# Kernel optimization log

Measured on AMD Instinct MI355X. Metric: run time of the kernel, lower is better.

The kernel has to match this reference:

```python
import jax, jax.numpy as jnp
import numpy as np

N_USERS = 50000
N_ITEMS = 100000
N_NODES = N_USERS + N_ITEMS
DIM = 64
N_EDGES = 1200000
N_LAYERS = 2


def setup_inputs() -> dict:
    key = jax.random.key(0)
    k1, k2, k3, k4, k5 = jax.random.split(key, 5)
    # xavier_uniform bound for an (n, dim) embedding: sqrt(6/(n+dim)); plain normal is fine for a correctness baseline
    user_emb = jax.random.normal(k1, (N_USERS, DIM), dtype=jnp.float32)
    item_emb = jax.random.normal(k2, (N_ITEMS, DIM), dtype=jnp.float32)
    edge_rows = jax.random.randint(k3, (N_EDGES,), 0, N_NODES, dtype=jnp.int32)
    edge_cols = jax.random.randint(k4, (N_EDGES,), 0, N_NODES, dtype=jnp.int32)
    edge_vals = jax.random.uniform(k5, (N_EDGES,), dtype=jnp.float32)
    return {
        "user_emb": user_emb,
        "item_emb": item_emb,
        "edge_rows": edge_rows,
        "edge_cols": edge_cols,
        "edge_vals": edge_vals,
    }


def _spmm(edge_rows, edge_cols, edge_vals, emb):
    # out[r] = sum over edges e with row r of vals[e] * emb[cols[e]]
    msgs = emb[edge_cols] * edge_vals[:, None]          # [E, dim]
    return jax.ops.segment_sum(msgs, edge_rows, num_segments=N_NODES)


def reference(user_emb, item_emb, edge_rows, edge_cols, edge_vals):
    emb = jnp.concatenate([user_emb, item_emb], axis=0)  # [N, dim]
    acc = emb
    e = emb
    for _ in range(N_LAYERS):
        e = _spmm(edge_rows, edge_cols, edge_vals, e)
        acc = acc + e
    out = acc / jnp.float32(N_LAYERS + 1)               # mean over [emb0, emb1, emb2]
    return out[:N_USERS], out[N_USERS:]
```

## Files before the change

### kernel.cpp

```cpp
#include <hip/hip_runtime.h>
#include <hip/hip_fp16.h>

#define N_USERS 50000
#define N_ITEMS 100000
#define N_NODES (N_USERS + N_ITEMS)
#define DIM 64
#define D2  (DIM / 2)
#define NCB 64
#define CROWS ((N_NODES + NCB - 1) / NCB)
#define CAP 24576
#define CHUNK 4096
#define SC 10

__global__ void init_kernel(const float4* __restrict__ user,
                            const float4* __restrict__ item,
                            uint2* __restrict__ buf0,
                            int* __restrict__ gcur,
                            int nUser4, int nTotal4) {
    int stride = gridDim.x * blockDim.x;
    int t0 = blockIdx.x * blockDim.x + threadIdx.x;
    for (int i = t0; i < nTotal4; i += stride) {
        float4 v = (i < nUser4) ? user[i] : item[i - nUser4];
        __half2 h0 = __floats2half2_rn(v.x, v.y);
        __half2 h1 = __floats2half2_rn(v.z, v.w);
        uint2 o;
        o.x = *(const unsigned int*)&h0;
        o.y = *(const unsigned int*)&h1;
        buf0[i] = o;
    }
    for (int i = t0; i < NCB; i += stride) gcur[i] = i * CAP;
}

__global__ __launch_bounds__(256) void binA_kernel(const int* __restrict__ rows,
                                                   const int* __restrict__ cols,
                                                   const float* __restrict__ vals,
                                                   int* __restrict__ gcur,
                                                   uint2* __restrict__ temp, int nE) {
    __shared__ uint2 stage[CHUNK];
    __shared__ int hist[NCB], off0[NCB], cur[NCB], gbase[NCB];
    int beg = blockIdx.x * CHUNK;
    int end = beg + CHUNK; if (end > nE) end = nE;
    for (int b = threadIdx.x; b < NCB; b += 256) hist[b] = 0;
    __syncthreads();
    for (int i = beg + threadIdx.x; i < end; i += 256) {
        int r = __builtin_nontemporal_load(rows + i);
        atomicAdd(&hist[r / CROWS], 1);
    }
    __syncthreads();
    if (threadIdx.x == 0) {
        int s = 0;
        for (int b = 0; b < NCB; ++b) { off0[b] = s; cur[b] = s; s += hist[b]; }
    }
    __syncthreads();
    for (int i = beg + threadIdx.x; i < end; i += 256) {
        int   r = rows[i];
        int   c = __builtin_nontemporal_load(cols + i);
        float v = __builtin_nontemporal_load(vals + i);
        int  cb = r / CROWS;
        int pos = atomicAdd(&cur[cb], 1);
        uint2 p;
        p.x = (unsigned)c | ((unsigned)(r - cb * CROWS) << 18);
        p.y = __float_as_uint(v);
        stage[pos] = p;
    }
    __syncthreads();
    for (int b = threadIdx.x; b < NCB; b += 256)
        gbase[b] = hist[b] ? atomicAdd(&gcur[b], hist[b]) : 0;
    __syncthreads();
    int wv = threadIdx.x >> 6, ln = threadIdx.x & 63;
    for (int b = wv; b < NCB; b += 4) {
        int len = hist[b], o0 = off0[b], gb = gbase[b];
        for (int j = ln; j < len; j += 64) temp[gb + j] = stage[o0 + j];
    }
}

__global__ __launch_bounds__(256) void binB_kernel(const int* __restrict__ gcur,
                                                   const uint2* __restrict__ temp,
                                                   float2* __restrict__ ebuf,
                                                   int* __restrict__ row_start) {
    __shared__ int rcnt[CROWS];
    __shared__ int rcur[CROWS];
    __shared__ int partial[256];
    __shared__ int csum[NCB];
    __shared__ int cstart_s;
    int b = blockIdx.x;
    int t = threadIdx.x;
    if (t < NCB) csum[t] = gcur[t] - t * CAP;
    __syncthreads();
    if (t == 0) {
        int s = 0;
        for (int j = 0; j < b; ++j) s += csum[j];
        cstart_s = s;
    }
    for (int i = t; i < CROWS; i += 256) rcnt[i] = 0;
    __syncthreads();
    int cnt_b  = csum[b];
    int cstart = cstart_s;
    int base   = b * CAP;
    for (int i = t; i < cnt_b; i += 256)
        atomicAdd(&rcnt[temp[base + i].x >> 18], 1);
    __syncthreads();
    int s = 0;
    #pragma unroll
    for (int k = 0; k < SC; ++k) {
        int idx = t * SC + k;
        if (idx < CROWS) { int v = rcnt[idx]; rcnt[idx] = s; s += v; }
    }
    partial[t] = s;
    __syncthreads();
    if (t == 0) {
        int s2 = 0;
        for (int j = 0; j < 256; ++j) { int v = partial[j]; partial[j] = s2; s2 += v; }
    }
    __syncthreads();
    int add = partial[t];
    #pragma unroll
    for (int k = 0; k < SC; ++k) {
        int idx = t * SC + k;
        if (idx < CROWS) rcnt[idx] += add;
    }
    __syncthreads();
    for (int i = t; i < CROWS; i += 256) {
        int gr = b * CROWS + i;
        if (gr < N_NODES) row_start[gr] = cstart + rcnt[i];
        rcur[i] = rcnt[i];
    }
    if (b == NCB - 1 && t == 0) row_start[N_NODES] = cstart + cnt_b;
    __syncthreads();
    for (int i = t; i < cnt_b; i += 256) {
        uint2 p  = temp[base + i];
        int   rl = p.x >> 18;
        int  pos = cstart + atomicAdd(&rcur[rl], 1);
        ebuf[pos] = make_float2(__int_as_float((int)(p.x & 0x3FFFF)),
                                __uint_as_float(p.y));
    }
}

#define GBLOCK2(U)                                                             \
    {                                                                          \
        float2 ev[U];                                                          \
        _Pragma("unroll") for (int j = 0; j < U; ++j) ev[j] = edges[i + j];    \
        __half2 sv[U];                                                         \
        _Pragma("unroll") for (int j = 0; j < U; ++j)                          \
            sv[j] = src2[(size_t)__float_as_int(ev[j].x) * D2 + d2];           \
        _Pragma("unroll") for (int j = 0; j < U; ++j) {                        \
            float2 s = __half22float2(sv[j]);                                  \
            acc.x = fmaf(ev[j].y, s.x, acc.x);                                 \
            acc.y = fmaf(ev[j].y, s.y, acc.y);                                 \
        }                                                                      \
        i += U;                                                                \
    }

template <int MODE>
__global__ void spmm_csr2_kernel(const int* __restrict__ row_start,
                                 const int* __restrict__ row_end,
                                 const float2* __restrict__ edges,
                                 const __half2* __restrict__ src2,
                                 __half2* __restrict__ dst2,
                                 const float2* __restrict__ user2,
                                 const float2* __restrict__ item2,
                                 const __half2* __restrict__ prev2,
                                 float2* __restrict__ out2) {
    int wave = (blockIdx.x * blockDim.x + threadIdx.x) >> 6;
    int lane = threadIdx.x & 63;
    int half = lane >> 5;
    int d2   = lane & 31;
    int row  = wave * 2 + half;
    if (row >= N_NODES) return;
    int i   = row_start[row];
    int end = row_end[row];
    float2 acc = make_float2(0.f, 0.f);

    while (end - i >= 8) GBLOCK2(8)
    if (end - i >= 4)    GBLOCK2(4)
    if (end - i >= 2)    GBLOCK2(2)
    if (end - i >= 1)    GBLOCK2(1)

    size_t o = (size_t)row * D2 + d2;
    if (MODE == 0) {
        dst2[o] = __floats2half2_rn(acc.x, acc.y);
    } else {
        float2 emb = (row < N_USERS) ? user2[o]
                                     : item2[o - (size_t)N_USERS * D2];
        float2 p = __half22float2(prev2[o]);
        out2[o] = make_float2((emb.x + p.x + acc.x) * (1.0f / 3.0f),
                              (emb.y + p.y + acc.y) * (1.0f / 3.0f));
    }
}

extern "C" void kernel_launch(void* const* d_in, const int* in_sizes, int n_in,
                              void* d_out, int out_size, void* d_ws, size_t ws_size,
                              hipStream_t stream) {
    const float* user = (const float*)d_in[0];
    const float* item = (const float*)d_in[1];
    const int*   rows = (const int*)d_in[2];
    const int*   cols = (const int*)d_in[3];
    const float* vals = (const float*)d_in[4];
    float* out = (float*)d_out;

    const int    nEdges = in_sizes[2];
    const size_t nNodeF = (size_t)N_NODES * DIM;

    __half* buf0      = (__half*)d_ws;
    __half* buf1      = buf0 + nNodeF;
    float2* ebuf      = (float2*)(buf1 + nNodeF);
    uint2*  temp      = (uint2*)(ebuf + nEdges);
    int*    gcur      = (int*)(temp + (size_t)NCB * CAP);
    int*    row_start = gcur + NCB;

    const int n4      = (int)(nNodeF / 4);
    const int nUser4  = N_USERS * DIM / 4;
    const int aBlocks = (nEdges + CHUNK - 1) / CHUNK;
    const int nWaves  = (N_NODES + 1) / 2;
    const int spmmBlocks = (nWaves + 3) / 4;

    init_kernel<<<512, 256, 0, stream>>>((const float4*)user, (const float4*)item,
                                         (uint2*)buf0, gcur, nUser4, n4);
    binA_kernel<<<aBlocks, 256, 0, stream>>>(rows, cols, vals, gcur, temp, nEdges);
    binB_kernel<<<NCB, 256, 0, stream>>>(gcur, temp, ebuf, row_start);
    spmm_csr2_kernel<0><<<spmmBlocks, 256, 0, stream>>>(row_start, row_start + 1,
                                                        ebuf,
                                                        (const __half2*)buf0,
                                                        (__half2*)buf1,
                                                        nullptr, nullptr, nullptr,
                                                        nullptr);
    spmm_csr2_kernel<1><<<spmmBlocks, 256, 0, stream>>>(row_start, row_start + 1,
                                                        ebuf,
                                                        (const __half2*)buf1,
                                                        nullptr,
                                                        (const float2*)user,
                                                        (const float2*)item,
                                                        (const __half2*)buf1,
                                                        (float2*)out);
}
```

Measured before the change: 248.4 us.

## Use finer binning, parallel scans, and quarter-wave rows with 8-byte gathers in SpMM

Raises the coarse bin count from 64 to 256 so binB runs 256 blocks of 512 threads instead of 64 blocks, giving more parallelism and smaller per-bin shared-memory scans. Serial single-thread prefix sums in both binning kernels become Hillis-Steele parallel scans. The SpMM kernel now processes four rows per wave, with 16 lanes each gathering 4 halves (8 bytes), which halves the lanes per row and doubles the gather width. A bin could overflow if the random distribution puts more than 6144 edges in it (the expected count is about 4700), and there is less edge-level parallelism per row.

New measurement: 208.8 us. -15.9%, faster.

```diff
diff --git a/kernel.cpp b/kernel.cpp
--- a/kernel.cpp
+++ b/kernel.cpp
@@ -5,12 +5,10 @@
 #define N_ITEMS 100000
 #define N_NODES (N_USERS + N_ITEMS)
 #define DIM 64
-#define D2  (DIM / 2)
-#define NCB 64
+#define NCB 256
 #define CROWS ((N_NODES + NCB - 1) / NCB)
-#define CAP 24576
+#define CAP 6144
 #define CHUNK 4096
-#define SC 10
 
 __global__ void init_kernel(const float4* __restrict__ user,
                             const float4* __restrict__ item,
@@ -38,21 +36,30 @@
                                                    uint2* __restrict__ temp, int nE) {
     __shared__ uint2 stage[CHUNK];
     __shared__ int hist[NCB], off0[NCB], cur[NCB], gbase[NCB];
+    __shared__ int s0[NCB], s1[NCB];
+    int t = threadIdx.x;
     int beg = blockIdx.x * CHUNK;
     int end = beg + CHUNK; if (end > nE) end = nE;
-    for (int b = threadIdx.x; b < NCB; b += 256) hist[b] = 0;
-    __syncthreads();
-    for (int i = beg + threadIdx.x; i < end; i += 256) {
+    hist[t] = 0;
+    __syncthreads();
+    for (int i = beg + t; i < end; i += 256) {
         int r = __builtin_nontemporal_load(rows + i);
         atomicAdd(&hist[r / CROWS], 1);
     }
     __syncthreads();
-    if (threadIdx.x == 0) {
-        int s = 0;
-        for (int b = 0; b < NCB; ++b) { off0[b] = s; cur[b] = s; s += hist[b]; }
-    }
-    __syncthreads();
-    for (int i = beg + threadIdx.x; i < end; i += 256) {
+    s0[t] = hist[t];
+    __syncthreads();
+    int* sA = s0; int* sB = s1;
+    for (int off = 1; off < NCB; off <<= 1) {
+        int v = sA[t] + (t >= off ? sA[t - off] : 0);
+        sB[t] = v;
+        __syncthreads();
+        int* tmp = sA; sA = sB; sB = tmp;
+    }
+    off0[t] = sA[t] - hist[t];
+    cur[t]  = off0[t];
+    __syncthreads();
+    for (int i = beg + t; i < end; i += 256) {
         int   r = rows[i];
         int   c = __builtin_nontemporal_load(cols + i);
         float v = __builtin_nontemporal_load(vals + i);
@@ -64,70 +71,73 @@
         stage[pos] = p;
     }
     __syncthreads();
-    for (int b = threadIdx.x; b < NCB; b += 256)
-        gbase[b] = hist[b] ? atomicAdd(&gcur[b], hist[b]) : 0;
-    __syncthreads();
-    int wv = threadIdx.x >> 6, ln = threadIdx.x & 63;
-    for (int b = wv; b < NCB; b += 4) {
+    gbase[t] = hist[t] ? atomicAdd(&gcur[t], hist[t]) : 0;
+    __syncthreads();
+    int hw = t >> 5, ln = t & 31;
+    for (int b = hw; b < NCB; b += 8) {
         int len = hist[b], o0 = off0[b], gb = gbase[b];
-        for (int j = ln; j < len; j += 64) temp[gb + j] = stage[o0 + j];
-    }
-}
-
-__global__ __launch_bounds__(256) void binB_kernel(const int* __restrict__ gcur,
+        for (int j = ln; j < len; j += 32) temp[gb + j] = stage[o0 + j];
+    }
+}
+
+__global__ __launch_bounds__(512) void binB_kernel(const int* __restrict__ gcur,
                                                    const uint2* __restrict__ temp,
                                                    float2* __restrict__ ebuf,
                                                    int* __restrict__ row_start) {
     __shared__ int rcnt[CROWS];
     __shared__ int rcur[CROWS];
-    __shared__ int partial[256];
-    __shared__ int csum[NCB];
-    __shared__ int cstart_s;
+    __shared__ int p0[512], p1[512];
+    __shared__ int cs0[NCB], cs1[NCB];
     int b = blockIdx.x;
     int t = threadIdx.x;
-    if (t < NCB) csum[t] = gcur[t] - t * CAP;
-    __syncthreads();
-    if (t == 0) {
-        int s = 0;
-        for (int j = 0; j < b; ++j) s += csum[j];
-        cstart_s = s;
-    }
-    for (int i = t; i < CROWS; i += 256) rcnt[i] = 0;
-    __syncthreads();
-    int cnt_b  = csum[b];
-    int cstart = cstart_s;
-    int base   = b * CAP;
-    for (int i = t; i < cnt_b; i += 256)
+    if (t < NCB) cs0[t] = gcur[t] - t * CAP;
+    __syncthreads();
+    int* cA = cs0; int* cB = cs1;
+    for (int off = 1; off < NCB; off <<= 1) {
+        int v = 0;
+        if (t < NCB) v = cA[t] + (t >= off ? cA[t - off] : 0);
+        if (t < NCB) cB[t] = v;
+        __syncthreads();
+        int* tmp = cA; cA = cB; cB = tmp;
+    }
+    int cstart = (b == 0) ? 0 : cA[b - 1];
+    int cnt_b  = cA[b] - cstart;
+    for (int i = t; i < CROWS; i += 512) rcnt[i] = 0;
+    __syncthreads();
+    int base = b * CAP;
+    for (int i = t; i < cnt_b; i += 512)
         atomicAdd(&rcnt[temp[base + i].x >> 18], 1);
     __syncthreads();
     int s = 0;
     #pragma unroll
-    for (int k = 0; k < SC; ++k) {
-        int idx = t * SC + k;
+    for (int k = 0; k < 2; ++k) {
+        int idx = t * 2 + k;
         if (idx < CROWS) { int v = rcnt[idx]; rcnt[idx] = s; s += v; }
     }
-    partial[t] = s;
-    __syncthreads();
-    if (t == 0) {
-        int s2 = 0;
-        for (int j = 0; j < 256; ++j) { int v = partial[j]; partial[j] = s2; s2 += v; }
-    }
-    __syncthreads();
-    int add = partial[t];
+    p0[t] = s;
+    __syncthreads();
+    int* pA = p0; int* pB = p1;
+    for (int off = 1; off < 512; off <<= 1) {
+        int v = pA[t] + (t >= off ? pA[t - off] : 0);
+        pB[t] = v;
+        __syncthreads();
+        int* tmp = pA; pA = pB; pB = tmp;
+    }
+    int add = (t == 0) ? 0 : pA[t - 1];
     #pragma unroll
-    for (int k = 0; k < SC; ++k) {
-        int idx = t * SC + k;
+    for (int k = 0; k < 2; ++k) {
+        int idx = t * 2 + k;
         if (idx < CROWS) rcnt[idx] += add;
     }
     __syncthreads();
-    for (int i = t; i < CROWS; i += 256) {
+    for (int i = t; i < CROWS; i += 512) {
         int gr = b * CROWS + i;
         if (gr < N_NODES) row_start[gr] = cstart + rcnt[i];
         rcur[i] = rcnt[i];
     }
     if (b == NCB - 1 && t == 0) row_start[N_NODES] = cstart + cnt_b;
     __syncthreads();
-    for (int i = t; i < cnt_b; i += 256) {
+    for (int i = t; i < cnt_b; i += 512) {
         uint2 p  = temp[base + i];
         int   rl = p.x >> 18;
         int  pos = cstart + atomicAdd(&rcur[rl], 1);
@@ -136,55 +146,68 @@
     }
 }
 
-#define GBLOCK2(U)                                                             \
+#define GBLOCK4(U)                                                             \
     {                                                                          \
         float2 ev[U];                                                          \
         _Pragma("unroll") for (int j = 0; j < U; ++j) ev[j] = edges[i + j];    \
-        __half2 sv[U];                                                         \
+        uint2 sv[U];                                                           \
         _Pragma("unroll") for (int j = 0; j < U; ++j)                          \
-            sv[j] = src2[(size_t)__float_as_int(ev[j].x) * D2 + d2];           \
+            sv[j] = src4[(size_t)__float_as_int(ev[j].x) * 16 + l16];          \
         _Pragma("unroll") for (int j = 0; j < U; ++j) {                        \
-            float2 s = __half22float2(sv[j]);                                  \
-            acc.x = fmaf(ev[j].y, s.x, acc.x);                                 \
-            acc.y = fmaf(ev[j].y, s.y, acc.y);                                 \
+            float2 a0 = __half22float2(*(__half2*)&sv[j].x);                   \
+            float2 a1 = __half22float2(*(__half2*)&sv[j].y);                   \
+            float v = ev[j].y;                                                 \
+            acc.x = fmaf(v, a0.x, acc.x);                                      \
+            acc.y = fmaf(v, a0.y, acc.y);                                      \
+            acc.z = fmaf(v, a1.x, acc.z);                                      \
+            acc.w = fmaf(v, a1.y, acc.w);                                      \
         }                                                                      \
         i += U;                                                                \
     }
 
 template <int MODE>
-__global__ void spmm_csr2_kernel(const int* __restrict__ row_start,
-                                 const int* __restrict__ row_end,
+__global__ void spmm_csr4_kernel(const int* __restrict__ row_start,
                                  const float2* __restrict__ edges,
-                                 const __half2* __restrict__ src2,
-                                 __half2* __restrict__ dst2,
-                                 const float2* __restrict__ user2,
-                                 const float2* __restrict__ item2,
-                                 const __half2* __restrict__ prev2,
-                                 float2* __restrict__ out2) {
+                                 const uint2* __restrict__ src4,
+                                 uint2* __restrict__ dst4,
+                                 const float4* __restrict__ user4,
+                                 const float4* __restrict__ item4,
+                                 const uint2* __restrict__ prev4,
+                                 float4* __restrict__ out4) {
     int wave = (blockIdx.x * blockDim.x + threadIdx.x) >> 6;
     int lane = threadIdx.x & 63;
-    int half = lane >> 5;
-    int d2   = lane & 31;
-    int row  = wave * 2 + half;
+    int sub  = lane >> 4;
+    int l16  = lane & 15;
+    int row  = wave * 4 + sub;
     if (row >= N_NODES) return;
     int i   = row_start[row];
-    int end = row_end[row];
-    float2 acc = make_float2(0.f, 0.f);
-
-    while (end - i >= 8) GBLOCK2(8)
-    if (end - i >= 4)    GBLOCK2(4)
-    if (end - i >= 2)    GBLOCK2(2)
-    if (end - i >= 1)    GBLOCK2(1)
-
-    size_t o = (size_t)row * D2 + d2;
+    int end = row_start[row + 1];
+    float4 acc = make_float4(0.f, 0.f, 0.f, 0.f);
+
+    while (end - i >= 8) GBLOCK4(8)
+    if (end - i >= 4)    GBLOCK4(4)
+    if (end - i >= 2)    GBLOCK4(2)
+    if (end - i >= 1)    GBLOCK4(1)
+
+    size_t o = (size_t)row * 16 + l16;
     if (MODE == 0) {
-        dst2[o] = __floats2half2_rn(acc.x, acc.y);
+        __half2 h0 = __floats2half2_rn(acc.x, acc.y);
+        __half2 h1 = __floats2half2_rn(acc.z, acc.w);
+        uint2 p;
+        p.x = *(unsigned*)&h0;
+        p.y = *(unsigned*)&h1;
+        dst4[o] = p;
     } else {
-        float2 emb = (row < N_USERS) ? user2[o]
-                                     : item2[o - (size_t)N_USERS * D2];
-        float2 p = __half22float2(prev2[o]);
-        out2[o] = make_float2((emb.x + p.x + acc.x) * (1.0f / 3.0f),
-                              (emb.y + p.y + acc.y) * (1.0f / 3.0f));
+        float4 emb = (row < N_USERS) ? user4[o]
+                                     : item4[o - (size_t)N_USERS * 16];
+        uint2 pv = prev4[o];
+        float2 q0 = __half22float2(*(__half2*)&pv.x);
+        float2 q1 = __half22float2(*(__half2*)&pv.y);
+        const float s = 1.0f / 3.0f;
+        out4[o] = make_float4((emb.x + q0.x + acc.x) * s,
+                              (emb.y + q0.y + acc.y) * s,
+                              (emb.z + q1.x + acc.z) * s,
+                              (emb.w + q1.y + acc.w) * s);
     }
 }
 
@@ -211,25 +234,23 @@
     const int n4      = (int)(nNodeF / 4);
     const int nUser4  = N_USERS * DIM / 4;
     const int aBlocks = (nEdges + CHUNK - 1) / CHUNK;
-    const int nWaves  = (N_NODES + 1) / 2;
+    const int nWaves  = (N_NODES + 3) / 4;
     const int spmmBlocks = (nWaves + 3) / 4;
 
     init_kernel<<<512, 256, 0, stream>>>((const float4*)user, (const float4*)item,
                                          (uint2*)buf0, gcur, nUser4, n4);
     binA_kernel<<<aBlocks, 256, 0, stream>>>(rows, cols, vals, gcur, temp, nEdges);
-    binB_kernel<<<NCB, 256, 0, stream>>>(gcur, temp, ebuf, row_start);
-    spmm_csr2_kernel<0><<<spmmBlocks, 256, 0, stream>>>(row_start, row_start + 1,
-                                                        ebuf,
-                                                        (const __half2*)buf0,
-                                                        (__half2*)buf1,
+    binB_kernel<<<NCB, 512, 0, stream>>>(gcur, temp, ebuf, row_start);
+    spmm_csr4_kernel<0><<<spmmBlocks, 256, 0, stream>>>(row_start, ebuf,
+                                                        (const uint2*)buf0,
+                                                        (uint2*)buf1,
                                                         nullptr, nullptr, nullptr,
                                                         nullptr);
-    spmm_csr2_kernel<1><<<spmmBlocks, 256, 0, stream>>>(row_start, row_start + 1,
-                                                        ebuf,
-                                                        (const __half2*)buf1,
+    spmm_csr4_kernel<1><<<spmmBlocks, 256, 0, stream>>>(row_start, ebuf,
+                                                        (const uint2*)buf1,
                                                         nullptr,
-                                                        (const float2*)user,
-                                                        (const float2*)item,
-                                                        (const __half2*)buf1,
-                                                        (float2*)out);
-}
+                                                        (const float4*)user,
+                                                        (const float4*)item,
+                                                        (const uint2*)buf1,
+                                                        (float4*)out);
+}
```
